# Kernel optimization log

Hardware: AMD Instinct MI355X
Metric: run time of the kernel (lower is better)

The kernel has to match this reference:

```python
import jax, jax.numpy as jnp
import numpy as np
from jax import lax


def setup_inputs() -> dict:
    key = jax.random.key(0)
    x = jax.random.normal(key, (8, 1, 2048, 2048), dtype=jnp.float32)
    return {"x": x}


def reference(x):
    # torch.median over the whole tensor returns the LOWER median for even counts:
    # k-th smallest element with k = (n - 1) // 2.
    n = x.size
    med = jnp.sort(x.ravel())[(n - 1) // 2]

    # Threshold everything <= median to zero.
    thr = jnp.where(x > med, x, jnp.zeros_like(x))

    # 7x7 max pool, stride 1, padding 3 (torch pads with -inf), output same HxW.
    maxed = lax.reduce_window(
        thr,
        -jnp.inf,
        lax.max,
        window_dimensions=(1, 1, 7, 7),
        window_strides=(1, 1, 1, 1),
        padding=((0, 0), (0, 0), (3, 3), (3, 3)),
    )

    # Keep only local maxima (entries equal to their window max), scaled by score.
    out = jnp.where(thr == maxed, thr, jnp.zeros_like(thr))
    return out
```

## Files before the change

kernel.cpp:

```cpp
#include <hip/hip_runtime.h>
#include <math.h>

#define IMG_H 2048
#define IMG_W 2048
#define TX 64
#define TY 32
#define HALO 3
#define TILE_H (TY + 2 * HALO)
#define SIN_STR 76
#define SHM_STR 68
#define CAND_CAP (1u << 20)
#define CBUF 1024
#define SEL_CAP 28672

__device__ __forceinline__ float4 fmax4(float4 a, float4 b) {
    return make_float4(fmaxf(a.x, b.x), fmaxf(a.y, b.y), fmaxf(a.z, b.z), fmaxf(a.w, b.w));
}

typedef float __attribute__((ext_vector_type(4))) fvec4;
__device__ __forceinline__ void nt_store4(float* p, float4 v) {
    fvec4 w; w.x = v.x; w.y = v.y; w.z = v.z; w.w = v.w;
    __builtin_nontemporal_store(w, (fvec4*)p);
}

__device__ __forceinline__ unsigned f2key(unsigned u) {
    unsigned mask = (unsigned)(((int)u >> 31)) | 0x80000000u;
    return u ^ mask;
}

__device__ __forceinline__ bool is_covered(const unsigned* __restrict__ ctrl, unsigned k) {
    unsigned cb = ctrl[7];
    unsigned ca = ctrl[2]; if (ca > CAND_CAP) ca = CAND_CAP;
    return (ctrl[3] == 0u) && (k >= cb) && (k - cb < ca);
}

__device__ __forceinline__ unsigned block_exscan(unsigned val, unsigned* tmp) {
    const int t = threadIdx.x;
    tmp[t] = val;
    __syncthreads();
#pragma unroll
    for (int off = 1; off < 256; off <<= 1) {
        unsigned v = (t >= off) ? tmp[t - off] : 0u;
        __syncthreads();
        tmp[t] += v;
        __syncthreads();
    }
    return tmp[t] - val;
}

template <int C>
__device__ __forceinline__ void find_crossing(const unsigned* bins, unsigned k,
                                              unsigned* tmp, unsigned* res) {
    unsigned s = 0;
#pragma unroll
    for (int j = 0; j < C; ++j) s += bins[threadIdx.x * C + j];
    unsigned ex = block_exscan(s, tmp);
    if (k >= ex && k < ex + s) {
        unsigned cum = ex;
        int b = threadIdx.x * C;
        while (cum + bins[b] <= k) { cum += bins[b]; ++b; }
        res[0] = (unsigned)b;
        res[1] = k - cum;
    }
    __syncthreads();
}

__global__ __launch_bounds__(256) void pass1_kernel(
        const float4* __restrict__ x, int n4, unsigned* __restrict__ ctrl,
        unsigned* __restrict__ candA, float W) {
    __shared__ unsigned cbuf[CBUF];
    __shared__ unsigned red[256];
    __shared__ unsigned ccnt, sbase, scnt;
    if (threadIdx.x == 0) ccnt = 0;
    __syncthreads();
    const float lo = -W, hi = W;
    unsigned cnt = 0;
    const int stride = gridDim.x * blockDim.x;
    for (int i = blockIdx.x * blockDim.x + threadIdx.x; i < n4; i += stride) {
        float4 v = x[i];
        cnt += (unsigned)(v.x <= lo) + (unsigned)(v.y <= lo) +
               (unsigned)(v.z <= lo) + (unsigned)(v.w <= lo);
        if (v.x > lo && v.x < hi) { unsigned p = atomicAdd(&ccnt, 1u); if (p < CBUF) cbuf[p] = f2key(__float_as_uint(v.x)); }
        if (v.y > lo && v.y < hi) { unsigned p = atomicAdd(&ccnt, 1u); if (p < CBUF) cbuf[p] = f2key(__float_as_uint(v.y)); }
        if (v.z > lo && v.z < hi) { unsigned p = atomicAdd(&ccnt, 1u); if (p < CBUF) cbuf[p] = f2key(__float_as_uint(v.z)); }
        if (v.w > lo && v.w < hi) { unsigned p = atomicAdd(&ccnt, 1u); if (p < CBUF) cbuf[p] = f2key(__float_as_uint(v.w)); }
    }
    red[threadIdx.x] = cnt;
    __syncthreads();
#pragma unroll
    for (int off = 128; off > 0; off >>= 1) {
        if (threadIdx.x < off) red[threadIdx.x] += red[threadIdx.x + off];
        __syncthreads();
    }
    if (threadIdx.x == 0) atomicAdd(&ctrl[7], red[0]);
    if (threadIdx.x == 0) {
        unsigned c = ccnt;
        if (c > CBUF) { c = CBUF; atomicOr(&ctrl[3], 1u); }
        unsigned base = atomicAdd(&ctrl[2], c);
        if (base + c > CAND_CAP) {
            atomicOr(&ctrl[3], 1u);
            c = base < CAND_CAP ? CAND_CAP - base : 0;
        }
        sbase = base; scnt = c;
    }
    __syncthreads();
    for (unsigned i = threadIdx.x; i < scnt; i += 256) candA[sbase + i] = cbuf[i];
}

__global__ __launch_bounds__(256) void fallback_hist_kernel(
        const float4* __restrict__ x, int n4, unsigned* __restrict__ ghist,
        const unsigned* __restrict__ ctrl, unsigned k) {
    if (is_covered(ctrl, k)) return;
    __shared__ unsigned h[4 * 2048];
    const int wave = threadIdx.x >> 6;
    unsigned* hw = &h[wave * 2048];
    for (int i = threadIdx.x; i < 4 * 2048; i += 256) h[i] = 0;
    __syncthreads();
    const int stride = gridDim.x * blockDim.x;
    for (int i = blockIdx.x * blockDim.x + threadIdx.x; i < n4; i += stride) {
        float4 v = x[i];
        atomicAdd(&hw[f2key(__float_as_uint(v.x)) >> 21], 1u);
        atomicAdd(&hw[f2key(__float_as_uint(v.y)) >> 21], 1u);
        atomicAdd(&hw[f2key(__float_as_uint(v.z)) >> 21], 1u);
        atomicAdd(&hw[f2key(__float_as_uint(v.w)) >> 21], 1u);
    }
    __syncthreads();
    for (int b = threadIdx.x; b < 2048; b += 256) {
        unsigned s = h[b] + h[2048 + b] + h[4096 + b] + h[6144 + b];
        if (s) atomicAdd(&ghist[b], s);
    }
}

__global__ __launch_bounds__(256) void find_bucket_kernel(
        const unsigned* __restrict__ ghist, unsigned k, unsigned* __restrict__ ctrl) {
    if (is_covered(ctrl, k)) return;
    __shared__ unsigned lh[2048];
    __shared__ unsigned tmp[256];
    __shared__ unsigned res[2];
    for (int i = threadIdx.x; i < 2048; i += 256) lh[i] = ghist[i];
    __syncthreads();
    find_crossing<8>(lh, k, tmp, res);
    if (threadIdx.x == 0) { ctrl[0] = res[0]; ctrl[1] = res[1]; }
}

__global__ __launch_bounds__(256) void compact_fallback_kernel(
        const float4* __restrict__ x, int n4, unsigned* __restrict__ ctrl,
        unsigned* __restrict__ candB, unsigned k) {
    if (is_covered(ctrl, k)) return;
    const unsigned bucket = ctrl[0];
    const int stride = gridDim.x * blockDim.x;
    for (int i = blockIdx.x * blockDim.x + threadIdx.x; i < n4; i += stride) {
        float4 v = x[i];
        unsigned ks[4] = { f2key(__float_as_uint(v.x)), f2key(__float_as_uint(v.y)),
                           f2key(__float_as_uint(v.z)), f2key(__float_as_uint(v.w)) };
#pragma unroll
        for (int j = 0; j < 4; ++j)
            if ((ks[j] >> 21) == bucket) {
                unsigned p = atomicAdd(&ctrl[5], 1u);
                if (p < CAND_CAP) candB[p] = ks[j];
            }
    }
}

__global__ __launch_bounds__(256) void final_select_kernel(
        unsigned* __restrict__ ctrl, const unsigned* __restrict__ candA,
        const unsigned* __restrict__ candB, float* __restrict__ medp, unsigned k) {
    __shared__ unsigned keys[SEL_CAP];
    __shared__ unsigned h2[2048];
    __shared__ unsigned tmp[256];
    __shared__ unsigned res[2];
    const int t = threadIdx.x;
    if (is_covered(ctrl, k)) {
        unsigned M = ctrl[2];
        const unsigned r = k - ctrl[7];
        const bool staged = (M <= SEL_CAP);
        if (staged) {
            unsigned M4 = M >> 2;
            const uint4* c4 = (const uint4*)candA;
            for (unsigned i = t; i < M4; i += 256) {
                uint4 q = c4[i];
                keys[4 * i] = q.x; keys[4 * i + 1] = q.y;
                keys[4 * i + 2] = q.z; keys[4 * i + 3] = q.w;
            }
            for (unsigned i = (M4 << 2) + t; i < M; i += 256) keys[i] = candA[i];
        }
        const unsigned* src = staged ? (const unsigned*)keys : candA;
        __syncthreads();
        for (unsigned i = t; i < 2048; i += 256) h2[i] = 0;
        __syncthreads();
        for (unsigned i = t; i < M; i += 256) atomicAdd(&h2[src[i] >> 21], 1u);
        __syncthreads();
        find_crossing<8>(h2, r, tmp, res);
        const unsigned b1 = res[0];
        const unsigned r1 = res[1];
        __syncthreads();
        for (unsigned i = t; i < 2048; i += 256) h2[i] = 0;
        __syncthreads();
        for (unsigned i = t; i < M; i += 256) {
            unsigned key = src[i];
            if ((key >> 21) == b1) atomicAdd(&h2[(key >> 10) & 0x7FFu], 1u);
        }
        __syncthreads();
        find_crossing<8>(h2, r1, tmp, res);
        const unsigned pref = (b1 << 11) | res[0];
        const unsigned r2 = res[1];
        __syncthreads();
        for (unsigned i = t; i < 1024; i += 256) h2[i] = 0;
        __syncthreads();
        for (unsigned i = t; i < M; i += 256) {
            unsigned key = src[i];
            if ((key >> 10) == pref) atomicAdd(&h2[key & 0x3FFu], 1u);
        }
        __syncthreads();
        find_crossing<4>(h2, r2, tmp, res);
        if (t == 0) {
            unsigned key = (pref << 10) | res[0];
            unsigned u = (key & 0x80000000u) ? (key ^ 0x80000000u) : ~key;
            *medp = __uint_as_float(u);
        }
    } else {
        unsigned M = ctrl[5]; if (M > CAND_CAP) M = CAND_CAP;
        const unsigned bucket = ctrl[0];
        const unsigned r = ctrl[1];
        for (int i = t; i < 2048; i += 256) h2[i] = 0;
        __syncthreads();
        for (unsigned i = t; i < M; i += 256) {
            unsigned key = candB[i];
            if ((key >> 21) == bucket) atomicAdd(&h2[(key >> 10) & 0x7FFu], 1u);
        }
        __syncthreads();
        find_crossing<8>(h2, r, tmp, res);
        const unsigned pref = (bucket << 11) | res[0];
        const unsigned r2 = res[1];
        __syncthreads();
        for (int i = t; i < 1024; i += 256) h2[i] = 0;
        __syncthreads();
        for (unsigned i = t; i < M; i += 256) {
            unsigned key = candB[i];
            if ((key >> 10) == pref) atomicAdd(&h2[key & 0x3FFu], 1u);
        }
        __syncthreads();
        find_crossing<4>(h2, r2, tmp, res);
        if (t == 0) {
            unsigned key = (pref << 10) | res[0];
            unsigned u = (key & 0x80000000u) ? (key ^ 0x80000000u) : ~key;
            *medp = __uint_as_float(u);
        }
    }
}

__global__ __launch_bounds__(256, 6) void nms_kernel(const float* __restrict__ x,
                                                     float* __restrict__ out,
                                                     const float* __restrict__ medp) {
    __shared__ __align__(16) float sin_[TILE_H * SIN_STR];
    __shared__ __align__(16) float shm[TILE_H * SHM_STR];
    const float med = *medp;
    const int tx0 = blockIdx.x * TX;
    const int ty0 = blockIdx.y * TY;
    const size_t ib = (size_t)blockIdx.z * (size_t)(IMG_H * IMG_W);
    const float* img = x + ib;
    float* oimg = out + ib;
    const bool colsafe = (tx0 >= 4) && (tx0 + 68 <= IMG_W);

    for (int task = threadIdx.x; task < TILE_H * 18; task += 256) {
        int rr = task / 18;
        int c4 = task - rr * 18;
        int gy = ty0 + rr - HALO;
        int gx0 = tx0 - 4 + c4 * 4;
        float4 v;
        if ((unsigned)gy < (unsigned)IMG_H) {
            if (colsafe) {
                v = *(const float4*)(img + (size_t)gy * IMG_W + gx0);
                v.x = (v.x > med) ? v.x : 0.0f;
                v.y = (v.y > med) ? v.y : 0.0f;
                v.z = (v.z > med) ? v.z : 0.0f;
                v.w = (v.w > med) ? v.w : 0.0f;
            } else {
                float c[4];
#pragma unroll
                for (int j = 0; j < 4; ++j) {
                    int gx = gx0 + j;
                    if ((unsigned)gx < (unsigned)IMG_W) {
                        float xv = img[(size_t)gy * IMG_W + gx];
                        c[j] = (xv > med) ? xv : 0.0f;
                    } else c[j] = -INFINITY;
                }
                v = make_float4(c[0], c[1], c[2], c[3]);
            }
        } else {
            v = make_float4(-INFINITY, -INFINITY, -INFINITY, -INFINITY);
        }
        *(float4*)&sin_[rr * SIN_STR + c4 * 4] = v;
    }
    __syncthreads();

    for (int task = threadIdx.x; task < TILE_H * 4; task += 256) {
        int rr = task >> 2;
        int s = task & 3;
        int c0 = s * 16;
        const float* p = &sin_[rr * SIN_STR + c0];
        float v[24];
#pragma unroll
        for (int b = 0; b < 6; ++b) {
            float4 q = *(const float4*)(p + 4 * b);
            v[4 * b] = q.x; v[4 * b + 1] = q.y; v[4 * b + 2] = q.z; v[4 * b + 3] = q.w;
        }
        float m2[22];
#pragma unroll
        for (int j = 1; j <= 21; ++j) m2[j] = fmaxf(v[j], v[j + 1]);
        float m4[20];
#pragma unroll
        for (int j = 1; j <= 19; ++j) m4[j] = fmaxf(m2[j], m2[j + 2]);
        float o[16];
#pragma unroll
        for (int j = 0; j < 16; ++j) o[j] = fmaxf(m4[j + 1], m4[j + 4]);
        float* q = &shm[rr * SHM_STR + c0];
#pragma unroll
        for (int b = 0; b < 4; ++b)
            *(float4*)(q + 4 * b) = make_float4(o[4 * b], o[4 * b + 1], o[4 * b + 2], o[4 * b + 3]);
    }
    __syncthreads();

    {
        const int col4 = threadIdx.x & 15;
        const int r0 = (threadIdx.x >> 4) * 2;
        float4 v[8];
#pragma unroll
        for (int j = 0; j < 8; ++j) v[j] = *(const float4*)&shm[(r0 + j) * SHM_STR + col4 * 4];
        float4 m2[7];
#pragma unroll
        for (int j = 0; j < 7; ++j) m2[j] = fmax4(v[j], v[j + 1]);
        float4 m4[5];
#pragma unroll
        for (int j = 0; j < 5; ++j) m4[j] = fmax4(m2[j], m2[j + 2]);
        float4 ma = fmax4(m4[0], m4[3]);
        float4 mb = fmax4(m4[1], m4[4]);
        float4 ta = *(const float4*)&sin_[(r0 + HALO) * SIN_STR + col4 * 4 + 4];
        float4 tb = *(const float4*)&sin_[(r0 + 1 + HALO) * SIN_STR + col4 * 4 + 4];
        float4 oa = make_float4((ta.x == ma.x) ? ta.x : 0.0f, (ta.y == ma.y) ? ta.y : 0.0f,
                                (ta.z == ma.z) ? ta.z : 0.0f, (ta.w == ma.w) ? ta.w : 0.0f);
        float4 ob = make_float4((tb.x == mb.x) ? tb.x : 0.0f, (tb.y == mb.y) ? tb.y : 0.0f,
                                (tb.z == mb.z) ? tb.z : 0.0f, (tb.w == mb.w) ? tb.w : 0.0f);
        nt_store4(oimg + (size_t)(ty0 + r0) * IMG_W + tx0 + col4 * 4, oa);
        nt_store4(oimg + (size_t)(ty0 + r0 + 1) * IMG_W + tx0 + col4 * 4, ob);
    }
}

extern "C" void kernel_launch(void* const* d_in, const int* in_sizes, int n_in,
                              void* d_out, int out_size, void* d_ws, size_t ws_size,
                              hipStream_t stream) {
    const float* x = (const float*)d_in[0];
    float* out = (float*)d_out;
    const int n = in_sizes[0];
    const int n4 = n / 4;
    const unsigned k = (unsigned)((n - 1) / 2);

    unsigned char* ws = (unsigned char*)d_ws;
    unsigned* ghist = (unsigned*)ws;
    unsigned* ctrl = (unsigned*)(ws + 2048 * 4);
    float* medp = (float*)(ctrl + 8);
    unsigned* candA = (unsigned*)(ws + 2048 * 4 + 64);
    unsigned* candB = candA + CAND_CAP;
    const size_t reserved = 2048 * 4 + 64;

    hipMemsetAsync(d_ws, 0, reserved, stream);

    const float W = 0.001f;

    pass1_kernel<<<1024, 256, 0, stream>>>((const float4*)x, n4, ctrl, candA, W);
    fallback_hist_kernel<<<1024, 256, 0, stream>>>((const float4*)x, n4, ghist, ctrl, k);
    find_bucket_kernel<<<1, 256, 0, stream>>>(ghist, k, ctrl);
    compact_fallback_kernel<<<1024, 256, 0, stream>>>((const float4*)x, n4, ctrl, candB, k);
    final_select_kernel<<<1, 256, 0, stream>>>(ctrl, candA, candB, medp, k);

    dim3 grid(IMG_W / TX, IMG_H / TY, n / (IMG_H * IMG_W));
    nms_kernel<<<grid, 256, 0, stream>>>(x, out, medp);
}
```

Baseline: 326.9 us.

## Use linear value bins and rank-count selection in single-block median select

The single-block select step now bins candidates by value linearly across the narrow window instead of by high key bits, gathers the crossing bin into shared memory, and picks the median by brute-force rank counting when that bin is small. This is meant to replace three sequential histogram passes over the candidates with one histogram plus a short quadratic pass. Pass 1 also compares integer keys instead of floats, and the NMS output stores change from nontemporal to regular vector stores. The radix fallback stays for bins that overflow the buffer, and the quadratic pass could get costly if a bin holds many candidates.

```diff
diff --git a/kernel.cpp b/kernel.cpp
--- a/kernel.cpp
+++ b/kernel.cpp
@@ -12,20 +12,32 @@
 #define CAND_CAP (1u << 20)
 #define CBUF 1024
 #define SEL_CAP 28672
+#define CSEL 4096
 
 __device__ __forceinline__ float4 fmax4(float4 a, float4 b) {
     return make_float4(fmaxf(a.x, b.x), fmaxf(a.y, b.y), fmaxf(a.z, b.z), fmaxf(a.w, b.w));
-}
-
-typedef float __attribute__((ext_vector_type(4))) fvec4;
-__device__ __forceinline__ void nt_store4(float* p, float4 v) {
-    fvec4 w; w.x = v.x; w.y = v.y; w.z = v.z; w.w = v.w;
-    __builtin_nontemporal_store(w, (fvec4*)p);
 }
 
 __device__ __forceinline__ unsigned f2key(unsigned u) {
     unsigned mask = (unsigned)(((int)u >> 31)) | 0x80000000u;
     return u ^ mask;
+}
+static inline unsigned f2key_host(float f) {
+    union { float f; unsigned u; } c; c.f = f;
+    unsigned mask = (unsigned)(((int)c.u >> 31)) | 0x80000000u;
+    return c.u ^ mask;
+}
+
+__device__ __forceinline__ float key2f(unsigned key) {
+    unsigned u = (key & 0x80000000u) ? (key ^ 0x80000000u) : ~key;
+    return __uint_as_float(u);
+}
+
+__device__ __forceinline__ unsigned linbin(unsigned key, float W, float scale) {
+    float p = (key2f(key) + W) * scale;
+    int b = (int)p;
+    b = b < 0 ? 0 : (b > 2047 ? 2047 : b);
+    return (unsigned)b;
 }
 
 __device__ __forceinline__ bool is_covered(const unsigned* __restrict__ ctrl, unsigned k) {
@@ -67,23 +79,26 @@
 
 __global__ __launch_bounds__(256) void pass1_kernel(
         const float4* __restrict__ x, int n4, unsigned* __restrict__ ctrl,
-        unsigned* __restrict__ candA, float W) {
+        unsigned* __restrict__ candA, unsigned keyLo, unsigned keyHi) {
     __shared__ unsigned cbuf[CBUF];
     __shared__ unsigned red[256];
     __shared__ unsigned ccnt, sbase, scnt;
     if (threadIdx.x == 0) ccnt = 0;
     __syncthreads();
-    const float lo = -W, hi = W;
     unsigned cnt = 0;
     const int stride = gridDim.x * blockDim.x;
     for (int i = blockIdx.x * blockDim.x + threadIdx.x; i < n4; i += stride) {
         float4 v = x[i];
-        cnt += (unsigned)(v.x <= lo) + (unsigned)(v.y <= lo) +
-               (unsigned)(v.z <= lo) + (unsigned)(v.w <= lo);
-        if (v.x > lo && v.x < hi) { unsigned p = atomicAdd(&ccnt, 1u); if (p < CBUF) cbuf[p] = f2key(__float_as_uint(v.x)); }
-        if (v.y > lo && v.y < hi) { unsigned p = atomicAdd(&ccnt, 1u); if (p < CBUF) cbuf[p] = f2key(__float_as_uint(v.y)); }
-        if (v.z > lo && v.z < hi) { unsigned p = atomicAdd(&ccnt, 1u); if (p < CBUF) cbuf[p] = f2key(__float_as_uint(v.z)); }
-        if (v.w > lo && v.w < hi) { unsigned p = atomicAdd(&ccnt, 1u); if (p < CBUF) cbuf[p] = f2key(__float_as_uint(v.w)); }
+        unsigned k0 = f2key(__float_as_uint(v.x));
+        unsigned k1 = f2key(__float_as_uint(v.y));
+        unsigned k2 = f2key(__float_as_uint(v.z));
+        unsigned k3 = f2key(__float_as_uint(v.w));
+        cnt += (unsigned)(k0 <= keyLo) + (unsigned)(k1 <= keyLo) +
+               (unsigned)(k2 <= keyLo) + (unsigned)(k3 <= keyLo);
+        if (k0 > keyLo && k0 < keyHi) { unsigned p = atomicAdd(&ccnt, 1u); if (p < CBUF) cbuf[p] = k0; }
+        if (k1 > keyLo && k1 < keyHi) { unsigned p = atomicAdd(&ccnt, 1u); if (p < CBUF) cbuf[p] = k1; }
+        if (k2 > keyLo && k2 < keyHi) { unsigned p = atomicAdd(&ccnt, 1u); if (p < CBUF) cbuf[p] = k2; }
+        if (k3 > keyLo && k3 < keyHi) { unsigned p = atomicAdd(&ccnt, 1u); if (p < CBUF) cbuf[p] = k3; }
     }
     red[threadIdx.x] = cnt;
     __syncthreads();
@@ -164,11 +179,14 @@
 
 __global__ __launch_bounds__(256) void final_select_kernel(
         unsigned* __restrict__ ctrl, const unsigned* __restrict__ candA,
-        const unsigned* __restrict__ candB, float* __restrict__ medp, unsigned k) {
+        const unsigned* __restrict__ candB, float* __restrict__ medp,
+        unsigned k, float W) {
     __shared__ unsigned keys[SEL_CAP];
+    __shared__ unsigned cbin[CSEL];
     __shared__ unsigned h2[2048];
     __shared__ unsigned tmp[256];
     __shared__ unsigned res[2];
+    __shared__ unsigned csize;
     const int t = threadIdx.x;
     if (is_covered(ctrl, k)) {
         unsigned M = ctrl[2];
@@ -185,38 +203,72 @@
             for (unsigned i = (M4 << 2) + t; i < M; i += 256) keys[i] = candA[i];
         }
         const unsigned* src = staged ? (const unsigned*)keys : candA;
-        __syncthreads();
+        if (t == 0) csize = 0;
+        const float scale = 1024.0f / W;
         for (unsigned i = t; i < 2048; i += 256) h2[i] = 0;
         __syncthreads();
-        for (unsigned i = t; i < M; i += 256) atomicAdd(&h2[src[i] >> 21], 1u);
+        for (unsigned i = t; i < M; i += 256) atomicAdd(&h2[linbin(src[i], W, scale)], 1u);
         __syncthreads();
         find_crossing<8>(h2, r, tmp, res);
-        const unsigned b1 = res[0];
-        const unsigned r1 = res[1];
-        __syncthreads();
-        for (unsigned i = t; i < 2048; i += 256) h2[i] = 0;
+        const unsigned b0 = res[0];
+        const unsigned r0 = res[1];
         __syncthreads();
         for (unsigned i = t; i < M; i += 256) {
             unsigned key = src[i];
-            if ((key >> 21) == b1) atomicAdd(&h2[(key >> 10) & 0x7FFu], 1u);
-        }
-        __syncthreads();
-        find_crossing<8>(h2, r1, tmp, res);
-        const unsigned pref = (b1 << 11) | res[0];
-        const unsigned r2 = res[1];
-        __syncthreads();
-        for (unsigned i = t; i < 1024; i += 256) h2[i] = 0;
-        __syncthreads();
-        for (unsigned i = t; i < M; i += 256) {
-            unsigned key = src[i];
-            if ((key >> 10) == pref) atomicAdd(&h2[key & 0x3FFu], 1u);
-        }
-        __syncthreads();
-        find_crossing<4>(h2, r2, tmp, res);
-        if (t == 0) {
-            unsigned key = (pref << 10) | res[0];
-            unsigned u = (key & 0x80000000u) ? (key ^ 0x80000000u) : ~key;
-            *medp = __uint_as_float(u);
+            if (linbin(key, W, scale) == b0) {
+                unsigned p = atomicAdd(&csize, 1u);
+                if (p < CSEL) cbin[p] = key;
+            }
+        }
+        __syncthreads();
+        const unsigned C = csize;
+        if (C <= CSEL) {
+            for (unsigned i = t; i < C; i += 256) {
+                unsigned key = cbin[i];
+                unsigned less = 0, eq = 0;
+                for (unsigned j = 0; j < C; ++j) {
+                    unsigned kj = cbin[j];
+                    less += (unsigned)(kj < key);
+                    eq += (unsigned)(kj == key);
+                }
+                if (less <= r0 && r0 < less + eq) res[0] = key;
+            }
+            __syncthreads();
+            if (t == 0) *medp = key2f(res[0]);
+        } else {
+            for (unsigned i = t; i < 2048; i += 256) h2[i] = 0;
+            __syncthreads();
+            for (unsigned i = t; i < M; i += 256) {
+                unsigned key = src[i];
+                if (linbin(key, W, scale) == b0) atomicAdd(&h2[key >> 21], 1u);
+            }
+            __syncthreads();
+            find_crossing<8>(h2, r0, tmp, res);
+            const unsigned b1 = res[0];
+            const unsigned r1 = res[1];
+            __syncthreads();
+            for (unsigned i = t; i < 2048; i += 256) h2[i] = 0;
+            __syncthreads();
+            for (unsigned i = t; i < M; i += 256) {
+                unsigned key = src[i];
+                if (linbin(key, W, scale) == b0 && (key >> 21) == b1)
+                    atomicAdd(&h2[(key >> 10) & 0x7FFu], 1u);
+            }
+            __syncthreads();
+            find_crossing<8>(h2, r1, tmp, res);
+            const unsigned pref = (b1 << 11) | res[0];
+            const unsigned r2 = res[1];
+            __syncthreads();
+            for (unsigned i = t; i < 1024; i += 256) h2[i] = 0;
+            __syncthreads();
+            for (unsigned i = t; i < M; i += 256) {
+                unsigned key = src[i];
+                if (linbin(key, W, scale) == b0 && (key >> 10) == pref)
+                    atomicAdd(&h2[key & 0x3FFu], 1u);
+            }
+            __syncthreads();
+            find_crossing<4>(h2, r2, tmp, res);
+            if (t == 0) *medp = key2f((pref << 10) | res[0]);
         }
     } else {
         unsigned M = ctrl[5]; if (M > CAND_CAP) M = CAND_CAP;
@@ -241,11 +293,7 @@
         }
         __syncthreads();
         find_crossing<4>(h2, r2, tmp, res);
-        if (t == 0) {
-            unsigned key = (pref << 10) | res[0];
-            unsigned u = (key & 0x80000000u) ? (key ^ 0x80000000u) : ~key;
-            *medp = __uint_as_float(u);
-        }
+        if (t == 0) *medp = key2f((pref << 10) | res[0]);
     }
 }
 
@@ -341,8 +389,8 @@
                                 (ta.z == ma.z) ? ta.z : 0.0f, (ta.w == ma.w) ? ta.w : 0.0f);
         float4 ob = make_float4((tb.x == mb.x) ? tb.x : 0.0f, (tb.y == mb.y) ? tb.y : 0.0f,
                                 (tb.z == mb.z) ? tb.z : 0.0f, (tb.w == mb.w) ? tb.w : 0.0f);
-        nt_store4(oimg + (size_t)(ty0 + r0) * IMG_W + tx0 + col4 * 4, oa);
-        nt_store4(oimg + (size_t)(ty0 + r0 + 1) * IMG_W + tx0 + col4 * 4, ob);
+        *(float4*)(oimg + (size_t)(ty0 + r0) * IMG_W + tx0 + col4 * 4) = oa;
+        *(float4*)(oimg + (size_t)(ty0 + r0 + 1) * IMG_W + tx0 + col4 * 4) = ob;
     }
 }
 
@@ -366,12 +414,14 @@
     hipMemsetAsync(d_ws, 0, reserved, stream);
 
     const float W = 0.001f;
-
-    pass1_kernel<<<1024, 256, 0, stream>>>((const float4*)x, n4, ctrl, candA, W);
+    const unsigned keyLo = f2key_host(-W);
+    const unsigned keyHi = f2key_host(W);
+
+    pass1_kernel<<<1024, 256, 0, stream>>>((const float4*)x, n4, ctrl, candA, keyLo, keyHi);
     fallback_hist_kernel<<<1024, 256, 0, stream>>>((const float4*)x, n4, ghist, ctrl, k);
     find_bucket_kernel<<<1, 256, 0, stream>>>(ghist, k, ctrl);
     compact_fallback_kernel<<<1024, 256, 0, stream>>>((const float4*)x, n4, ctrl, candB, k);
-    final_select_kernel<<<1, 256, 0, stream>>>(ctrl, candA, candB, medp, k);
+    final_select_kernel<<<1, 256, 0, stream>>>(ctrl, candA, candB, medp, k, W);
 
     dim3 grid(IMG_W / TX, IMG_H / TY, n / (IMG_H * IMG_W));
     nms_kernel<<<grid, 256, 0, stream>>>(x, out, medp);
```

Result: no change. 325.9 us (-0.3%).
